# Optimization experiments

Hardware: AMD Instinct MI355X
Metric: run time of the kernel (lower is better)

## Reference

```python
import jax, jax.numpy as jnp
from jax import lax
import numpy as np

NPOINT, RADIUS, NSAMPLE = 1024, 0.2, 32
MLP = [64, 64, 128]
IN_CH = 35  # 3 coord channels + 32 point features
EPS = 1e-5


def farthest_point_sample(xyz, npoint):
    # xyz: (B, N, 3) -> (B, npoint) int32. Deterministic start at index 0.
    B, N, _ = xyz.shape

    def step(carry, _):
        dist, farthest = carry  # (B,N), (B,)
        centroid = jnp.take_along_axis(xyz, farthest[:, None, None], axis=1)  # (B,1,3)
        d = jnp.sum((xyz - centroid) ** 2, axis=-1)  # (B,N)
        dist = jnp.minimum(dist, d)
        nxt = jnp.argmax(dist, axis=-1).astype(jnp.int32)
        return (dist, nxt), farthest

    init = (jnp.full((B, N), 1e10, xyz.dtype), jnp.zeros((B,), jnp.int32))
    _, idxs = lax.scan(step, init, None, length=npoint)
    return idxs.T  # (B, npoint)


def gather_points(points, idx):
    # points: (B, N, C); idx: (B, ...) int -> (B, ..., C)
    return jax.vmap(lambda p, i: p[i])(points, idx)


def query_ball_point(radius, nsample, xyz, new_xyz):
    # xyz: (B,N,3), new_xyz: (B,S,3) -> (B,S,nsample) int32
    B, N, _ = xyz.shape
    sqrdists = jnp.sum((new_xyz[:, :, None, :] - xyz[:, None, :, :]) ** 2, axis=-1)  # (B,S,N)
    group_idx = jnp.where(sqrdists > radius ** 2, N, jnp.arange(N, dtype=jnp.int32))
    group_idx = jnp.sort(group_idx, axis=-1)[:, :, :nsample]
    first = group_idx[:, :, :1]
    return jnp.where(group_idx == N, first, group_idx)


def sa_forward(xyz, points, params):
    B, N, C = xyz.shape
    fps_idx = farthest_point_sample(xyz, NPOINT)
    new_xyz = gather_points(xyz, fps_idx)  # (B,S,3)
    idx = query_ball_point(RADIUS, NSAMPLE, xyz, new_xyz)  # (B,S,K)
    grouped_xyz = gather_points(xyz, idx)  # (B,S,K,3)
    grouped_xyz_norm = grouped_xyz - new_xyz[:, :, None, :]
    grouped_points = gather_points(points, idx)  # (B,S,K,D)
    new_points = jnp.concatenate([grouped_xyz_norm, grouped_points], axis=-1)  # (B,S,K,Cin)
    x = new_points.transpose(0, 3, 2, 1)  # (B, Cin, K, S)
    for w, b, g, be in params:
        x = jnp.einsum('oi,biks->boks', w, x) + b[None, :, None, None]  # 1x1 conv
        mean = x.mean(axis=(0, 2, 3), keepdims=True)  # BatchNorm2d, training mode
        var = x.var(axis=(0, 2, 3), keepdims=True)
        x = (x - mean) / jnp.sqrt(var + EPS)
        x = jax.nn.relu(g[None, :, None, None] * x + be[None, :, None, None])
    new_points_out = x.max(axis=2)  # max over nsample -> (B, Cout, S)
    return new_xyz, new_points_out


def setup_inputs() -> dict:
    key = jax.random.key(0)
    ks = jax.random.split(key, 16)
    B, N, D = 16, 4096, 32
    inp = {
        'xyz': jax.random.uniform(ks[0], (B, N, 3), dtype=jnp.float32),
        'points': jax.random.normal(ks[1], (B, N, D), dtype=jnp.float32),
    }
    last = IN_CH
    for li, out_ch in enumerate(MLP):
        inp[f'w{li}'] = jax.random.normal(ks[2 + 4 * li], (out_ch, last), dtype=jnp.float32) * 0.05
        inp[f'b{li}'] = jnp.zeros((out_ch,), jnp.float32)
        inp[f'g{li}'] = jnp.ones((out_ch,), jnp.float32)
        inp[f'be{li}'] = jnp.zeros((out_ch,), jnp.float32)
        last = out_ch
    return inp


def reference(xyz, points, w0, b0, g0, be0, w1, b1, g1, be1, w2, b2, g2, be2):
    params = [(w0, b0, g0, be0), (w1, b1, g1, be1), (w2, b2, g2, be2)]
    return sa_forward(xyz, points, params)
```

## Files before the change

kernel.cpp:

```cpp
#include <hip/hip_runtime.h>
#include <stdint.h>

#pragma clang fp contract(off)

#define BATCH   16
#define NPTS    4096
#define NPOINT  1024
#define NSAMPLE 32
#define NPOS    (BATCH*NPOINT*NSAMPLE)
#define EPSV    1e-5f

typedef unsigned short ushort_t;
typedef unsigned int uint_t;
typedef unsigned long long u64;
typedef __attribute__((ext_vector_type(8))) short bf16x8;
typedef __attribute__((ext_vector_type(4))) float f32x4;
typedef __attribute__((ext_vector_type(2))) float f32x2;

__device__ inline ushort_t f2bf(float f) {
    uint_t u = __float_as_uint(f);
    u += 0x7fffu + ((u >> 16) & 1u);
    return (ushort_t)(u >> 16);
}
__device__ inline void unpack8(uint4 u, float* f) {
    f[0] = __uint_as_float(u.x << 16); f[1] = __uint_as_float(u.x & 0xffff0000u);
    f[2] = __uint_as_float(u.y << 16); f[3] = __uint_as_float(u.y & 0xffff0000u);
    f[4] = __uint_as_float(u.z << 16); f[5] = __uint_as_float(u.z & 0xffff0000u);
    f[6] = __uint_as_float(u.w << 16); f[7] = __uint_as_float(u.w & 0xffff0000u);
}

__global__ void zero_kernel(float* __restrict__ p, int n) {
    int i = blockIdx.x * blockDim.x + threadIdx.x;
    if (i < n) p[i] = 0.f;
}

#define DPP_MAX_STAGE(CTRL) do {                                              \
    uint_t _lo2 = __builtin_amdgcn_update_dpp(lo, lo, CTRL, 0xf, 0xf, false); \
    uint_t _hi2 = __builtin_amdgcn_update_dpp(hi, hi, CTRL, 0xf, 0xf, false); \
    u64 _o = ((u64)_hi2 << 32) | _lo2;                                        \
    u64 _v = ((u64)hi << 32) | lo;                                            \
    bool _g = _o > _v;                                                        \
    lo = _g ? _lo2 : lo; hi = _g ? _hi2 : hi;                                 \
} while (0)

__global__ __launch_bounds__(256) void fps_kernel(const float* __restrict__ xyz,
                                                  float* __restrict__ new_xyz) {
    __shared__ float4 lxyz[NPTS];
    __shared__ u64 wbest[2][4];
    __shared__ int fpsidx[NPOINT];
    const int b = blockIdx.x;
    const int tid = threadIdx.x;
    const float* base = xyz + (size_t)b * NPTS * 3;
    for (int n = tid; n < NPTS; n += 256) {
        lxyz[n] = make_float4(base[3 * n], base[3 * n + 1], base[3 * n + 2], 0.f);
    }
    __syncthreads();

    f32x2 px[8], py[8], pz[8], dist[8];
    uint_t lowc[16];
#pragma unroll
    for (int j = 0; j < 8; j++) {
        float4 v0 = lxyz[tid + (2 * j) * 256];
        float4 v1 = lxyz[tid + (2 * j + 1) * 256];
        px[j] = (f32x2){v0.x, v1.x};
        py[j] = (f32x2){v0.y, v1.y};
        pz[j] = (f32x2){v0.z, v1.z};
        dist[j] = (f32x2){1e10f, 1e10f};
        lowc[2 * j] = ~(uint_t)(tid + (2 * j) * 256);
        lowc[2 * j + 1] = ~(uint_t)(tid + (2 * j + 1) * 256);
    }
    if (tid == 0) fpsidx[0] = 0;
    int cur = 0;
    const int lane = tid & 63, wid = tid >> 6;

    for (int it = 1; it < NPOINT; ++it) {
        float4 c = lxyz[cur];
        const f32x2 cx = (f32x2){c.x, c.x};
        const f32x2 cy = (f32x2){c.y, c.y};
        const f32x2 cz = (f32x2){c.z, c.z};
        u64 t[8];
#pragma unroll
        for (int j = 0; j < 8; j++) {
            f32x2 dx = px[j] - cx;
            f32x2 dy = py[j] - cy;
            f32x2 dz = pz[j] - cz;
            f32x2 d = (dx * dx + dy * dy) + dz * dz;
            f32x2 nd = __builtin_elementwise_min(dist[j], d);
            dist[j] = nd;
            u64 e0 = ((u64)__float_as_uint(nd.x) << 32) | lowc[2 * j];
            u64 e1 = ((u64)__float_as_uint(nd.y) << 32) | lowc[2 * j + 1];
            t[j] = e0 > e1 ? e0 : e1;
        }
#pragma unroll
        for (int j = 0; j < 4; j++) { u64 o = t[j + 4]; t[j] = t[j] > o ? t[j] : o; }
        t[0] = t[0] > t[1] ? t[0] : t[1];
        t[2] = t[2] > t[3] ? t[2] : t[3];
        u64 v = t[0] > t[2] ? t[0] : t[2];

        uint_t lo = (uint_t)v, hi = (uint_t)(v >> 32);
        DPP_MAX_STAGE(0x111);
        DPP_MAX_STAGE(0x112);
        DPP_MAX_STAGE(0x114);
        DPP_MAX_STAGE(0x118);
        DPP_MAX_STAGE(0x142);
        DPP_MAX_STAGE(0x143);
        uint_t mlo = __builtin_amdgcn_readlane(lo, 63);
        uint_t mhi = __builtin_amdgcn_readlane(hi, 63);

        const int par = it & 1;
        if (lane == 0) wbest[par][wid] = ((u64)mhi << 32) | mlo;
        __syncthreads();
        u64 b0 = wbest[par][0], b1 = wbest[par][1];
        u64 b2 = wbest[par][2], b3 = wbest[par][3];
        u64 m01 = b0 > b1 ? b0 : b1;
        u64 m23 = b2 > b3 ? b2 : b3;
        u64 bb = m01 > m23 ? m01 : m23;
        cur = (int)(~(uint_t)bb) & (NPTS - 1);
        if (tid == 0) fpsidx[it] = cur;
    }
    __syncthreads();
    float* ob = new_xyz + (size_t)b * NPOINT * 3;
    for (int s = tid; s < NPOINT; s += 256) {
        float4 v = lxyz[fpsidx[s]];
        ob[3 * s + 0] = v.x; ob[3 * s + 1] = v.y; ob[3 * s + 2] = v.z;
    }
}

__global__ __launch_bounds__(256) void ballq_kernel(const float* __restrict__ xyz,
                                                    const float* __restrict__ new_xyz,
                                                    int* __restrict__ gidx) {
    const int gw = (int)((blockIdx.x * 256 + threadIdx.x) >> 6);
    const int lane = threadIdx.x & 63;
    const int b = gw / NPOINT, s = gw % NPOINT;
    const float* nb = new_xyz + ((size_t)b * NPOINT + s) * 3;
    const float cx = nb[0], cy = nb[1], cz = nb[2];
    const float* xb = xyz + (size_t)b * NPTS * 3;
    const float r2 = (float)(0.2 * 0.2);
    int cnt = 0;
    int first = -1;
    int* out = gidx + (size_t)gw * NSAMPLE;
    for (int j0 = 0; j0 < NPTS; j0 += 64) {
        int j = j0 + lane;
        float dx = __fsub_rn(xb[j * 3 + 0], cx);
        float dy = __fsub_rn(xb[j * 3 + 1], cy);
        float dz = __fsub_rn(xb[j * 3 + 2], cz);
        float d = __fadd_rn(__fadd_rn(__fmul_rn(dx, dx), __fmul_rn(dy, dy)),
                            __fmul_rn(dz, dz));
        bool pred = !(d > r2);
        u64 mask = __ballot(pred);
        if (first < 0 && mask != 0ull) first = j0 + (__ffsll((long long)mask) - 1);
        int before = __popcll(mask & ((1ull << lane) - 1ull));
        int slot = cnt + before;
        if (pred && slot < NSAMPLE) out[slot] = j;
        cnt += (int)__popcll(mask);
        if (cnt >= NSAMPLE) break;
    }
    if (cnt < NSAMPLE) {
        if (lane >= cnt && lane < NSAMPLE) out[lane] = first;
    }
}

__global__ __launch_bounds__(256) void conv1_mfma(const float* __restrict__ xyz,
                                                  const float* __restrict__ points,
                                                  const float* __restrict__ new_xyz,
                                                  const int* __restrict__ gidx,
                                                  const float* __restrict__ W,
                                                  const float* __restrict__ bias,
                                                  ushort_t* __restrict__ Y,
                                                  float* __restrict__ sums,
                                                  float* __restrict__ sq) {
    const int lane = threadIdx.x & 63, wid = threadIdx.x >> 6;
    const int l15 = lane & 15, quad = lane >> 4;
    const int p0 = blockIdx.x * 128 + wid * 32;

    bf16x8 Bp[4], Bx[4];
#pragma unroll
    for (int nt = 0; nt < 4; nt++) {
        const float* wr = W + (size_t)(nt * 16 + l15) * 35;
#pragma unroll
        for (int q = 0; q < 8; q++) Bp[nt][q] = (short)f2bf(wr[3 + quad * 8 + q]);
#pragma unroll
        for (int q = 0; q < 8; q++)
            Bx[nt][q] = (quad == 0 && q < 3) ? (short)f2bf(wr[q]) : (short)0;
    }
    f32x4 acc[2][4];
#pragma unroll
    for (int mt = 0; mt < 2; mt++)
#pragma unroll
        for (int nt = 0; nt < 4; nt++) acc[mt][nt] = (f32x4){0.f, 0.f, 0.f, 0.f};

#pragma unroll
    for (int mt = 0; mt < 2; mt++) {
        const int p = p0 + mt * 16 + l15;
        const int b = p >> 15, s = (p & 32767) >> 5;
        const int j = gidx[p];
        const float* pr = points + ((size_t)(b * NPTS + j)) * 32 + quad * 8;
        bf16x8 Ap, Ax;
#pragma unroll
        for (int q = 0; q < 8; q++) Ap[q] = (short)f2bf(pr[q]);
#pragma unroll
        for (int q = 0; q < 8; q++) Ax[q] = 0;
        const float* xp = xyz + ((size_t)(b * NPTS + j)) * 3;
        const float* nz = new_xyz + ((size_t)(b * NPOINT + s)) * 3;
        if (quad == 0) {
            Ax[0] = (short)f2bf(xp[0] - nz[0]);
            Ax[1] = (short)f2bf(xp[1] - nz[1]);
            Ax[2] = (short)f2bf(xp[2] - nz[2]);
        }
#pragma unroll
        for (int nt = 0; nt < 4; nt++) {
            acc[mt][nt] = __builtin_amdgcn_mfma_f32_16x16x32_bf16(Ap, Bp[nt], acc[mt][nt], 0, 0, 0);
            acc[mt][nt] = __builtin_amdgcn_mfma_f32_16x16x32_bf16(Ax, Bx[nt], acc[mt][nt], 0, 0, 0);
        }
    }
    float s_[4], q_[4];
#pragma unroll
    for (int nt = 0; nt < 4; nt++) { s_[nt] = 0.f; q_[nt] = 0.f; }
#pragma unroll
    for (int nt = 0; nt < 4; nt++) {
        const int ch = nt * 16 + l15;
        const float bs = bias[ch];
#pragma unroll
        for (int mt = 0; mt < 2; mt++) {
            const int pb = p0 + mt * 16 + quad * 4;
#pragma unroll
            for (int r = 0; r < 4; r++) {
                float x = acc[mt][nt][r] + bs;
                uint_t u = __float_as_uint(x);
                u += 0x7fffu + ((u >> 16) & 1u);
                Y[(size_t)(pb + r) * 64 + ch] = (ushort_t)(u >> 16);
                float v = __uint_as_float(u & 0xffff0000u);
                s_[nt] += v; q_[nt] += v * v;
            }
        }
    }
#pragma unroll
    for (int nt = 0; nt < 4; nt++) {
        s_[nt] += __shfl_xor(s_[nt], 16, 64); s_[nt] += __shfl_xor(s_[nt], 32, 64);
        q_[nt] += __shfl_xor(q_[nt], 16, 64); q_[nt] += __shfl_xor(q_[nt], 32, 64);
    }
    __shared__ float reds[4][4][16], redq[4][4][16];
    if (lane < 16) {
#pragma unroll
        for (int nt = 0; nt < 4; nt++) { reds[wid][nt][lane] = s_[nt]; redq[wid][nt][lane] = q_[nt]; }
    }
    __syncthreads();
    if (threadIdx.x < 16) {
#pragma unroll
        for (int nt = 0; nt < 4; nt++) {
            float ss = 0.f, qq = 0.f;
#pragma unroll
            for (int w = 0; w < 4; w++) { ss += reds[w][nt][threadIdx.x]; qq += redq[w][nt][threadIdx.x]; }
            atomicAdd(sums + nt * 16 + threadIdx.x, ss);
            atomicAdd(sq + nt * 16 + threadIdx.x, qq);
        }
    }
}

template <int IN, int OUT>
__global__ __launch_bounds__(256) void convN_mfma(const ushort_t* __restrict__ Yin,
                                                  const float* __restrict__ scale,
                                                  const float* __restrict__ shift,
                                                  const float* __restrict__ W,
                                                  const float* __restrict__ bias,
                                                  ushort_t* __restrict__ Yout,
                                                  float* __restrict__ sums,
                                                  float* __restrict__ sq) {
    constexpr int NT = OUT / 16;
    const int lane = threadIdx.x & 63, wid = threadIdx.x >> 6;
    const int l15 = lane & 15, quad = lane >> 4;
    const int p0 = blockIdx.x * 128 + wid * 32;

    float sc[2][8], sh[2][8];
#pragma unroll
    for (int kq = 0; kq < 2; kq++) {
        const int i0 = kq * 32 + quad * 8;
#pragma unroll
        for (int q = 0; q < 8; q++) { sc[kq][q] = scale[i0 + q]; sh[kq][q] = shift[i0 + q]; }
    }
    bf16x8 Bf[NT][2];
#pragma unroll
    for (int nt = 0; nt < NT; nt++)
#pragma unroll
        for (int kq = 0; kq < 2; kq++) {
            const float* wr = W + (size_t)(nt * 16 + l15) * IN + kq * 32 + quad * 8;
#pragma unroll
            for (int q = 0; q < 8; q++) Bf[nt][kq][q] = (short)f2bf(wr[q]);
        }

    bf16x8 Af[2][2];
#pragma unroll
    for (int mt = 0; mt < 2; mt++)
#pragma unroll
        for (int kq = 0; kq < 2; kq++) {
            const ushort_t* yr = Yin + (size_t)(p0 + mt * 16 + l15) * IN + kq * 32 + quad * 8;
            uint4 u = *(const uint4*)yr;
            float f[8]; unpack8(u, f);
#pragma unroll
            for (int q = 0; q < 8; q++) {
                float x = fmaxf(fmaf(f[q], sc[kq][q], sh[kq][q]), 0.f);
                Af[mt][kq][q] = (short)f2bf(x);
            }
        }

    f32x4 acc[2][NT];
#pragma unroll
    for (int mt = 0; mt < 2; mt++)
#pragma unroll
        for (int nt = 0; nt < NT; nt++) acc[mt][nt] = (f32x4){0.f, 0.f, 0.f, 0.f};
#pragma unroll
    for (int mt = 0; mt < 2; mt++)
#pragma unroll
        for (int nt = 0; nt < NT; nt++) {
            acc[mt][nt] = __builtin_amdgcn_mfma_f32_16x16x32_bf16(Af[mt][0], Bf[nt][0], acc[mt][nt], 0, 0, 0);
            acc[mt][nt] = __builtin_amdgcn_mfma_f32_16x16x32_bf16(Af[mt][1], Bf[nt][1], acc[mt][nt], 0, 0, 0);
        }
    float s_[NT], q_[NT];
#pragma unroll
    for (int nt = 0; nt < NT; nt++) { s_[nt] = 0.f; q_[nt] = 0.f; }
#pragma unroll
    for (int nt = 0; nt < NT; nt++) {
        const int ch = nt * 16 + l15;
        const float bs = bias[ch];
#pragma unroll
        for (int mt = 0; mt < 2; mt++) {
            const int pb = p0 + mt * 16 + quad * 4;
#pragma unroll
            for (int r = 0; r < 4; r++) {
                float x = acc[mt][nt][r] + bs;
                uint_t u = __float_as_uint(x);
                u += 0x7fffu + ((u >> 16) & 1u);
                Yout[(size_t)(pb + r) * OUT + ch] = (ushort_t)(u >> 16);
                float v = __uint_as_float(u & 0xffff0000u);
                s_[nt] += v; q_[nt] += v * v;
            }
        }
    }
#pragma unroll
    for (int nt = 0; nt < NT; nt++) {
        s_[nt] += __shfl_xor(s_[nt], 16, 64); s_[nt] += __shfl_xor(s_[nt], 32, 64);
        q_[nt] += __shfl_xor(q_[nt], 16, 64); q_[nt] += __shfl_xor(q_[nt], 32, 64);
    }
    __shared__ float reds[4][NT][16], redq[4][NT][16];
    if (lane < 16) {
#pragma unroll
        for (int nt = 0; nt < NT; nt++) { reds[wid][nt][lane] = s_[nt]; redq[wid][nt][lane] = q_[nt]; }
    }
    __syncthreads();
    if (threadIdx.x < 16) {
#pragma unroll
        for (int nt = 0; nt < NT; nt++) {
            float ss = 0.f, qq = 0.f;
#pragma unroll
            for (int w = 0; w < 4; w++) { ss += reds[w][nt][threadIdx.x]; qq += redq[w][nt][threadIdx.x]; }
            atomicAdd(sums + nt * 16 + threadIdx.x, ss);
            atomicAdd(sq + nt * 16 + threadIdx.x, qq);
        }
    }
}

__global__ void finalize_kernel(const float* __restrict__ sums, const float* __restrict__ sq,
                                const float* __restrict__ g, const float* __restrict__ be,
                                float* __restrict__ scale, float* __restrict__ shift, int OUT) {
    int c = threadIdx.x;
    if (c < OUT) {
        float mean = sums[c] * (1.f / (float)NPOS);
        float var = sq[c] * (1.f / (float)NPOS) - mean * mean;
        float inv = 1.f / sqrtf(var + EPSV);
        float sc = g[c] * inv;
        scale[c] = sc;
        shift[c] = be[c] - mean * sc;
    }
}

__global__ __launch_bounds__(256) void final_kernel(const ushort_t* __restrict__ Y3,
                                                    const float* __restrict__ scale,
                                                    const float* __restrict__ shift,
                                                    float* __restrict__ out) {
    const int b = blockIdx.x >> 5;
    const int stile = (blockIdx.x & 31) * 32;
    const int sl = threadIdx.x >> 3;
    const int oc = threadIdx.x & 7;
    const int s = stile + sl;
    const size_t base = ((size_t)(b * NPOINT + s)) * 32 * 128 + oc * 16;
    float vmax[16];
#pragma unroll
    for (int i = 0; i < 16; i++) vmax[i] = 0.f;
    for (int k = 0; k < 32; k++) {
        const ushort_t* yp = Y3 + base + (size_t)k * 128;
#pragma unroll
        for (int h = 0; h < 2; h++) {
            uint4 u = *(const uint4*)(yp + h * 8);
            float f[8];
            unpack8(u, f);
#pragma unroll
            for (int i = 0; i < 8; i++) {
                int o = oc * 16 + h * 8 + i;
                float v = fmaf(f[i], scale[o], shift[o]);
                vmax[h * 8 + i] = fmaxf(vmax[h * 8 + i], v);
            }
        }
    }
    __shared__ float res[32][130];
#pragma unroll
    for (int i = 0; i < 16; i++) res[sl][oc * 16 + i] = vmax[i];
    __syncthreads();
    const int so = threadIdx.x & 31;
    const int og = threadIdx.x >> 5;
#pragma unroll
    for (int r = 0; r < 16; r++) {
        int o = og * 16 + r;
        out[((size_t)(b * 128 + o)) * NPOINT + stile + so] = res[so][o];
    }
}

extern "C" void kernel_launch(void* const* d_in, const int* in_sizes, int n_in,
                              void* d_out, int out_size, void* d_ws, size_t ws_size,
                              hipStream_t stream) {
    const float* xyz = (const float*)d_in[0];
    const float* points = (const float*)d_in[1];
    const float* w0 = (const float*)d_in[2];
    const float* b0 = (const float*)d_in[3];
    const float* g0 = (const float*)d_in[4];
    const float* be0 = (const float*)d_in[5];
    const float* w1 = (const float*)d_in[6];
    const float* b1 = (const float*)d_in[7];
    const float* g1 = (const float*)d_in[8];
    const float* be1 = (const float*)d_in[9];
    const float* w2 = (const float*)d_in[10];
    const float* b2 = (const float*)d_in[11];
    const float* g2 = (const float*)d_in[12];
    const float* be2 = (const float*)d_in[13];

    float* out = (float*)d_out;
    float* new_xyz = out;
    float* final_out = out + BATCH * NPOINT * 3;

    char* ws = (char*)d_ws;
    const size_t MB = 1024u * 1024u;
    const size_t o_gidx = 0;
    const size_t o_y2 = 2 * MB;
    const size_t o_y13 = o_y2 + (size_t)NPOS * 64 * 2;
    const size_t o_stats = o_y13 + (size_t)NPOS * 128 * 2;
    const size_t o_params = o_stats + 2048;

    int* gidx = (int*)(ws + o_gidx);
    ushort_t* Y1 = (ushort_t*)(ws + o_y13);
    ushort_t* Y2 = (ushort_t*)(ws + o_y2);
    ushort_t* Y3 = (ushort_t*)(ws + o_y13);
    float* st = (float*)(ws + o_stats);
    float* sum1 = st + 0, *sq1 = st + 64;
    float* sum2 = st + 128, *sq2 = st + 192;
    float* sum3 = st + 256, *sq3 = st + 384;
    float* pr = (float*)(ws + o_params);
    float* scale1 = pr + 0, *shift1 = pr + 64;
    float* scale2 = pr + 128, *shift2 = pr + 192;
    float* scale3 = pr + 256, *shift3 = pr + 384;

    zero_kernel<<<1, 512, 0, stream>>>(st, 512);

    fps_kernel<<<BATCH, 256, 0, stream>>>(xyz, new_xyz);
    ballq_kernel<<<(BATCH * NPOINT) / 4, 256, 0, stream>>>(xyz, new_xyz, gidx);
    conv1_mfma<<<NPOS / 128, 256, 0, stream>>>(xyz, points, new_xyz, gidx, w0, b0, Y1, sum1, sq1);
    finalize_kernel<<<1, 128, 0, stream>>>(sum1, sq1, g0, be0, scale1, shift1, 64);
    convN_mfma<64, 64><<<NPOS / 128, 256, 0, stream>>>(Y1, scale1, shift1, w1, b1, Y2, sum2, sq2);
    finalize_kernel<<<1, 128, 0, stream>>>(sum2, sq2, g1, be1, scale2, shift2, 64);
    convN_mfma<64, 128><<<NPOS / 128, 256, 0, stream>>>(Y2, scale2, shift2, w2, b2, Y3, sum3, sq3);
    finalize_kernel<<<1, 128, 0, stream>>>(sum3, sq3, g2, be2, scale3, shift3, 128);
    final_kernel<<<BATCH * 32, 256, 0, stream>>>(Y3, scale3, shift3, final_out);
}
```

Before: 1.113 ms.

## Replace BN stat atomics with per-block partials and widen FPS to 512 threads

Each conv block now writes its per-channel sum and sum-of-squares to its own slot in a partials buffer, and a per-channel reduce_finalize kernel sums them. This removes the global float atomics, the zero-init kernel and the single-block finalize. FPS now runs with 512 threads per batch, so each thread holds half as many points. That shortens the serial per-iteration work, but the cross-wave reduction now spans 8 waves and the block is larger.

```diff
diff --git a/kernel.cpp b/kernel.cpp
--- a/kernel.cpp
+++ b/kernel.cpp
@@ -8,6 +8,7 @@
 #define NPOINT  1024
 #define NSAMPLE 32
 #define NPOS    (BATCH*NPOINT*NSAMPLE)
+#define NBLK    (NPOS/128)
 #define EPSV    1e-5f
 
 typedef unsigned short ushort_t;
@@ -27,11 +28,6 @@
     f[2] = __uint_as_float(u.y << 16); f[3] = __uint_as_float(u.y & 0xffff0000u);
     f[4] = __uint_as_float(u.z << 16); f[5] = __uint_as_float(u.z & 0xffff0000u);
     f[6] = __uint_as_float(u.w << 16); f[7] = __uint_as_float(u.w & 0xffff0000u);
-}
-
-__global__ void zero_kernel(float* __restrict__ p, int n) {
-    int i = blockIdx.x * blockDim.x + threadIdx.x;
-    if (i < n) p[i] = 0.f;
 }
 
 #define DPP_MAX_STAGE(CTRL) do {                                              \
@@ -43,31 +39,31 @@
     lo = _g ? _lo2 : lo; hi = _g ? _hi2 : hi;                                 \
 } while (0)
 
-__global__ __launch_bounds__(256) void fps_kernel(const float* __restrict__ xyz,
+__global__ __launch_bounds__(512) void fps_kernel(const float* __restrict__ xyz,
                                                   float* __restrict__ new_xyz) {
     __shared__ float4 lxyz[NPTS];
-    __shared__ u64 wbest[2][4];
+    __shared__ u64 wbest[2][8];
     __shared__ int fpsidx[NPOINT];
     const int b = blockIdx.x;
     const int tid = threadIdx.x;
     const float* base = xyz + (size_t)b * NPTS * 3;
-    for (int n = tid; n < NPTS; n += 256) {
+    for (int n = tid; n < NPTS; n += 512) {
         lxyz[n] = make_float4(base[3 * n], base[3 * n + 1], base[3 * n + 2], 0.f);
     }
     __syncthreads();
 
-    f32x2 px[8], py[8], pz[8], dist[8];
-    uint_t lowc[16];
-#pragma unroll
-    for (int j = 0; j < 8; j++) {
-        float4 v0 = lxyz[tid + (2 * j) * 256];
-        float4 v1 = lxyz[tid + (2 * j + 1) * 256];
+    f32x2 px[4], py[4], pz[4], dist[4];
+    uint_t lowc[8];
+#pragma unroll
+    for (int j = 0; j < 4; j++) {
+        float4 v0 = lxyz[tid + (2 * j) * 512];
+        float4 v1 = lxyz[tid + (2 * j + 1) * 512];
         px[j] = (f32x2){v0.x, v1.x};
         py[j] = (f32x2){v0.y, v1.y};
         pz[j] = (f32x2){v0.z, v1.z};
         dist[j] = (f32x2){1e10f, 1e10f};
-        lowc[2 * j] = ~(uint_t)(tid + (2 * j) * 256);
-        lowc[2 * j + 1] = ~(uint_t)(tid + (2 * j + 1) * 256);
+        lowc[2 * j] = ~(uint_t)(tid + (2 * j) * 512);
+        lowc[2 * j + 1] = ~(uint_t)(tid + (2 * j + 1) * 512);
     }
     if (tid == 0) fpsidx[0] = 0;
     int cur = 0;
@@ -78,9 +74,9 @@
         const f32x2 cx = (f32x2){c.x, c.x};
         const f32x2 cy = (f32x2){c.y, c.y};
         const f32x2 cz = (f32x2){c.z, c.z};
-        u64 t[8];
-#pragma unroll
-        for (int j = 0; j < 8; j++) {
+        u64 t[4];
+#pragma unroll
+        for (int j = 0; j < 4; j++) {
             f32x2 dx = px[j] - cx;
             f32x2 dy = py[j] - cy;
             f32x2 dz = pz[j] - cz;
@@ -91,8 +87,6 @@
             u64 e1 = ((u64)__float_as_uint(nd.y) << 32) | lowc[2 * j + 1];
             t[j] = e0 > e1 ? e0 : e1;
         }
-#pragma unroll
-        for (int j = 0; j < 4; j++) { u64 o = t[j + 4]; t[j] = t[j] > o ? t[j] : o; }
         t[0] = t[0] > t[1] ? t[0] : t[1];
         t[2] = t[2] > t[3] ? t[2] : t[3];
         u64 v = t[0] > t[2] ? t[0] : t[2];
@@ -110,17 +104,23 @@
         const int par = it & 1;
         if (lane == 0) wbest[par][wid] = ((u64)mhi << 32) | mlo;
         __syncthreads();
-        u64 b0 = wbest[par][0], b1 = wbest[par][1];
-        u64 b2 = wbest[par][2], b3 = wbest[par][3];
-        u64 m01 = b0 > b1 ? b0 : b1;
-        u64 m23 = b2 > b3 ? b2 : b3;
-        u64 bb = m01 > m23 ? m01 : m23;
+        u64 w0 = wbest[par][0], w1 = wbest[par][1];
+        u64 w2 = wbest[par][2], w3 = wbest[par][3];
+        u64 w4 = wbest[par][4], w5 = wbest[par][5];
+        u64 w6 = wbest[par][6], w7 = wbest[par][7];
+        u64 a0 = w0 > w1 ? w0 : w1;
+        u64 a1 = w2 > w3 ? w2 : w3;
+        u64 a2 = w4 > w5 ? w4 : w5;
+        u64 a3 = w6 > w7 ? w6 : w7;
+        a0 = a0 > a1 ? a0 : a1;
+        a2 = a2 > a3 ? a2 : a3;
+        u64 bb = a0 > a2 ? a0 : a2;
         cur = (int)(~(uint_t)bb) & (NPTS - 1);
         if (tid == 0) fpsidx[it] = cur;
     }
     __syncthreads();
     float* ob = new_xyz + (size_t)b * NPOINT * 3;
-    for (int s = tid; s < NPOINT; s += 256) {
+    for (int s = tid; s < NPOINT; s += 512) {
         float4 v = lxyz[fpsidx[s]];
         ob[3 * s + 0] = v.x; ob[3 * s + 1] = v.y; ob[3 * s + 2] = v.z;
     }
@@ -167,8 +167,8 @@
                                                   const float* __restrict__ W,
                                                   const float* __restrict__ bias,
                                                   ushort_t* __restrict__ Y,
-                                                  float* __restrict__ sums,
-                                                  float* __restrict__ sq) {
+                                                  float* __restrict__ part_s,
+                                                  float* __restrict__ part_q) {
     const int lane = threadIdx.x & 63, wid = threadIdx.x >> 6;
     const int l15 = lane & 15, quad = lane >> 4;
     const int p0 = blockIdx.x * 128 + wid * 32;
@@ -251,8 +251,9 @@
             float ss = 0.f, qq = 0.f;
 #pragma unroll
             for (int w = 0; w < 4; w++) { ss += reds[w][nt][threadIdx.x]; qq += redq[w][nt][threadIdx.x]; }
-            atomicAdd(sums + nt * 16 + threadIdx.x, ss);
-            atomicAdd(sq + nt * 16 + threadIdx.x, qq);
+            const int ch = nt * 16 + threadIdx.x;
+            part_s[(size_t)ch * NBLK + blockIdx.x] = ss;
+            part_q[(size_t)ch * NBLK + blockIdx.x] = qq;
         }
     }
 }
@@ -264,8 +265,8 @@
                                                   const float* __restrict__ W,
                                                   const float* __restrict__ bias,
                                                   ushort_t* __restrict__ Yout,
-                                                  float* __restrict__ sums,
-                                                  float* __restrict__ sq) {
+                                                  float* __restrict__ part_s,
+                                                  float* __restrict__ part_q) {
     constexpr int NT = OUT / 16;
     const int lane = threadIdx.x & 63, wid = threadIdx.x >> 6;
     const int l15 = lane & 15, quad = lane >> 4;
@@ -353,23 +354,39 @@
             float ss = 0.f, qq = 0.f;
 #pragma unroll
             for (int w = 0; w < 4; w++) { ss += reds[w][nt][threadIdx.x]; qq += redq[w][nt][threadIdx.x]; }
-            atomicAdd(sums + nt * 16 + threadIdx.x, ss);
-            atomicAdd(sq + nt * 16 + threadIdx.x, qq);
-        }
-    }
-}
-
-__global__ void finalize_kernel(const float* __restrict__ sums, const float* __restrict__ sq,
-                                const float* __restrict__ g, const float* __restrict__ be,
-                                float* __restrict__ scale, float* __restrict__ shift, int OUT) {
-    int c = threadIdx.x;
-    if (c < OUT) {
-        float mean = sums[c] * (1.f / (float)NPOS);
-        float var = sq[c] * (1.f / (float)NPOS) - mean * mean;
+            const int ch = nt * 16 + threadIdx.x;
+            part_s[(size_t)ch * NBLK + blockIdx.x] = ss;
+            part_q[(size_t)ch * NBLK + blockIdx.x] = qq;
+        }
+    }
+}
+
+__global__ __launch_bounds__(256) void reduce_finalize(const float* __restrict__ part_s,
+                                                       const float* __restrict__ part_q,
+                                                       const float* __restrict__ g,
+                                                       const float* __restrict__ be,
+                                                       float* __restrict__ scale,
+                                                       float* __restrict__ shift) {
+    const int ch = blockIdx.x;
+    const float* p1 = part_s + (size_t)ch * NBLK;
+    const float* p2 = part_q + (size_t)ch * NBLK;
+    float s = 0.f, q = 0.f;
+    for (int i = threadIdx.x; i < NBLK; i += 256) { s += p1[i]; q += p2[i]; }
+#pragma unroll
+    for (int m = 1; m < 64; m <<= 1) { s += __shfl_xor(s, m, 64); q += __shfl_xor(q, m, 64); }
+    __shared__ float ls[4], lq[4];
+    const int lane = threadIdx.x & 63, wid = threadIdx.x >> 6;
+    if (lane == 0) { ls[wid] = s; lq[wid] = q; }
+    __syncthreads();
+    if (threadIdx.x == 0) {
+        float ssum = ls[0] + ls[1] + ls[2] + ls[3];
+        float qsum = lq[0] + lq[1] + lq[2] + lq[3];
+        float mean = ssum * (1.f / (float)NPOS);
+        float var = qsum * (1.f / (float)NPOS) - mean * mean;
         float inv = 1.f / sqrtf(var + EPSV);
-        float sc = g[c] * inv;
-        scale[c] = sc;
-        shift[c] = be[c] - mean * sc;
+        float sc = g[ch] * inv;
+        scale[ch] = sc;
+        shift[ch] = be[ch] - mean * sc;
     }
 }
 
@@ -441,31 +458,27 @@
     const size_t o_gidx = 0;
     const size_t o_y2 = 2 * MB;
     const size_t o_y13 = o_y2 + (size_t)NPOS * 64 * 2;
-    const size_t o_stats = o_y13 + (size_t)NPOS * 128 * 2;
-    const size_t o_params = o_stats + 2048;
+    const size_t o_params = o_y13 + (size_t)NPOS * 128 * 2;
+    const size_t o_parts = o_params + 4096;
 
     int* gidx = (int*)(ws + o_gidx);
     ushort_t* Y1 = (ushort_t*)(ws + o_y13);
     ushort_t* Y2 = (ushort_t*)(ws + o_y2);
     ushort_t* Y3 = (ushort_t*)(ws + o_y13);
-    float* st = (float*)(ws + o_stats);
-    float* sum1 = st + 0, *sq1 = st + 64;
-    float* sum2 = st + 128, *sq2 = st + 192;
-    float* sum3 = st + 256, *sq3 = st + 384;
     float* pr = (float*)(ws + o_params);
     float* scale1 = pr + 0, *shift1 = pr + 64;
     float* scale2 = pr + 128, *shift2 = pr + 192;
     float* scale3 = pr + 256, *shift3 = pr + 384;
-
-    zero_kernel<<<1, 512, 0, stream>>>(st, 512);
-
-    fps_kernel<<<BATCH, 256, 0, stream>>>(xyz, new_xyz);
+    float* part_s = (float*)(ws + o_parts);
+    float* part_q = part_s + (size_t)128 * NBLK;
+
+    fps_kernel<<<BATCH, 512, 0, stream>>>(xyz, new_xyz);
     ballq_kernel<<<(BATCH * NPOINT) / 4, 256, 0, stream>>>(xyz, new_xyz, gidx);
-    conv1_mfma<<<NPOS / 128, 256, 0, stream>>>(xyz, points, new_xyz, gidx, w0, b0, Y1, sum1, sq1);
-    finalize_kernel<<<1, 128, 0, stream>>>(sum1, sq1, g0, be0, scale1, shift1, 64);
-    convN_mfma<64, 64><<<NPOS / 128, 256, 0, stream>>>(Y1, scale1, shift1, w1, b1, Y2, sum2, sq2);
-    finalize_kernel<<<1, 128, 0, stream>>>(sum2, sq2, g1, be1, scale2, shift2, 64);
-    convN_mfma<64, 128><<<NPOS / 128, 256, 0, stream>>>(Y2, scale2, shift2, w2, b2, Y3, sum3, sq3);
-    finalize_kernel<<<1, 128, 0, stream>>>(sum3, sq3, g2, be2, scale3, shift3, 128);
+    conv1_mfma<<<NBLK, 256, 0, stream>>>(xyz, points, new_xyz, gidx, w0, b0, Y1, part_s, part_q);
+    reduce_finalize<<<64, 256, 0, stream>>>(part_s, part_q, g0, be0, scale1, shift1);
+    convN_mfma<64, 64><<<NBLK, 256, 0, stream>>>(Y1, scale1, shift1, w1, b1, Y2, part_s, part_q);
+    reduce_finalize<<<64, 256, 0, stream>>>(part_s, part_q, g1, be1, scale2, shift2);
+    convN_mfma<64, 128><<<NBLK, 256, 0, stream>>>(Y2, scale2, shift2, w2, b2, Y3, part_s, part_q);
+    reduce_finalize<<<128, 256, 0, stream>>>(part_s, part_q, g2, be2, scale3, shift3);
     final_kernel<<<BATCH * 32, 256, 0, stream>>>(Y3, scale3, shift3, final_out);
 }
```

New measurement: 1.048 ms. -5.9%, faster.
